# Kernel tuning notes

Hardware: AMD Instinct MI355X
Metric: run time of the kernel (lower is better)

Reference implementation:

```python
import jax, jax.numpy as jnp
import numpy as np

B, M, F = 32, 32768, 256


def setup_inputs() -> dict:
    key = jax.random.key(0)
    ks = jax.random.split(key, 6)
    scale1 = 1.0 / np.sqrt(2 * F)
    scale2 = 1.0 / np.sqrt(F)
    return {
        "input_data": jax.random.normal(ks[0], (B, F), dtype=jnp.float32),
        "memory": jax.random.normal(ks[1], (M, F), dtype=jnp.float32),
        "W1": jax.random.uniform(ks[2], (F, 2 * F), jnp.float32, -scale1, scale1),
        "b1": jax.random.uniform(ks[3], (F,), jnp.float32, -scale1, scale1),
        "W2": jax.random.uniform(ks[4], (1, F), jnp.float32, -scale2, scale2),
        "b2": jax.random.uniform(ks[5], (1,), jnp.float32, -scale2, scale2),
        # threshold below 1/M so the conditional scatter-write path actually fires
        # (torch default 0.05 with random weights never writes for M=32768)
        "threshold": jnp.float32(1e-5),
    }


def reference(input_data, memory, W1, b1, W2, b2, threshold):
    # Linear on cat([x, mem]) splits into two independent matmuls.
    W1x, W1m = W1[:, :F], W1[:, F:]          # each [F, F]
    hx = input_data @ W1x.T                   # [B, F]
    hm = memory @ W1m.T                       # [M, F]
    h = jnp.tanh(hx[:, None, :] + hm[None, :, :] + b1)  # [B, M, F]
    scores = h @ W2[0] + b2[0]                # [B, M]
    weights = jax.nn.softmax(scores, axis=1)  # softmax over memory slots
    best = jnp.argmax(weights, axis=1)        # [B] winning slot per item
    maxw = jnp.max(weights, axis=1)           # [B]
    mask = maxw > threshold                   # write only if above threshold
    # Sequential loop semantics: later batch items overwrite earlier ones
    # at the same slot. last[s] = 1 + index of last masked writer to slot s.
    order = jnp.where(mask, jnp.arange(B, dtype=jnp.int32) + 1, 0)
    last = jax.ops.segment_max(order, best, num_segments=M)  # [M]
    last = jnp.maximum(last, 0)
    src = input_data[jnp.maximum(last - 1, 0)]               # [M, F]
    updated_memory = jnp.where((last > 0)[:, None], src, memory)
    return updated_memory
```

## Files before the change

### kernel.cpp

```cpp
#include <hip/hip_runtime.h>

#define FDIM 256
#define BDIM 32
#define MDIM 32768
#define NB   512

#define WS_EM    0
#define WS_EX    (WS_EM + MDIM*FDIM)
#define WS_W2N   (WS_EX + BDIM*FDIM)
#define WS_PMAX  (WS_W2N + FDIM)
#define WS_PSUM  (WS_PMAX + BDIM*NB)
#define WS_PARG  (WS_PSUM + BDIM*NB)
#define WS_WIN   (WS_PARG + BDIM*NB)
#define WS_BEST  (WS_WIN + 32)
#define WS_GMAX  (WS_BEST + 32)
#define WS_GSUM  (WS_GMAX + 32)
#define WS_GARG  (WS_GSUM + 32)
#define WS_WH    (WS_GARG + 32)
#define WS_WL    (WS_WH + 32768)

#define C2 2.8853900817779268f

typedef __attribute__((ext_vector_type(8))) short bf16x8;
typedef __attribute__((ext_vector_type(8))) unsigned short ushort8;
typedef __attribute__((ext_vector_type(4))) float f32x4;

__device__ inline unsigned short f2bf(float x) {
  unsigned u = __float_as_uint(x);
  return (unsigned short)((u + 0x7fffu + ((u >> 16) & 1u)) >> 16);
}
__device__ inline float bf2f(unsigned short h) {
  return __uint_as_float(((unsigned)h) << 16);
}

__global__ __launch_bounds__(256) void k1_prep(const float* __restrict__ input,
                                               const float* __restrict__ W1,
                                               const float* __restrict__ b1,
                                               const float* __restrict__ W2,
                                               float* __restrict__ Ex,
                                               float* __restrict__ w2n,
                                               unsigned short* __restrict__ wh,
                                               unsigned short* __restrict__ wl) {
  if (blockIdx.x < BDIM) {
    const int b = blockIdx.x, f = threadIdx.x;
    const float* in = input + b * FDIM;
    const float* w  = W1 + (size_t)f * 512;
    float acc = b1[f];
    #pragma unroll 8
    for (int k = 0; k < FDIM; k += 4) {
      float4 iv = *(const float4*)(in + k);
      float4 wv = *(const float4*)(w + k);
      acc = fmaf(iv.x, wv.x, acc); acc = fmaf(iv.y, wv.y, acc);
      acc = fmaf(iv.z, wv.z, acc); acc = fmaf(iv.w, wv.w, acc);
    }
    Ex[b * FDIM + f] = __builtin_amdgcn_exp2f(acc * C2);
    if (b == 0) w2n[f] = -2.0f * W2[f];
  } else {
    int id = ((blockIdx.x - BDIM) * 256 + threadIdx.x) * 4;
    int f = id >> 8, c = id & 255;
    float4 v = *(const float4*)(W1 + (size_t)f * 512 + 256 + c);
    float xs[4] = {v.x, v.y, v.z, v.w};
    #pragma unroll
    for (int e = 0; e < 4; ++e) {
      unsigned short h = f2bf(xs[e]);
      wh[id + e] = h;
      wl[id + e] = f2bf(xs[e] - bf2f(h));
    }
  }
}

__global__ __launch_bounds__(512, 4) void k23_fused(const float* __restrict__ mem,
                                                    const unsigned short* __restrict__ wh,
                                                    const unsigned short* __restrict__ wl,
                                                    const float* __restrict__ Ex,
                                                    const float* __restrict__ w2n,
                                                    float* __restrict__ pmax,
                                                    float* __restrict__ psum,
                                                    int* __restrict__ parg,
                                                    float* __restrict__ out) {
  __shared__ __align__(16) char smem[69632];
  unsigned short* AH = (unsigned short*)(smem);
  unsigned short* AL = (unsigned short*)(smem + 5120);
  unsigned short* BH = (unsigned short*)(smem + 10240);
  unsigned short* BL = (unsigned short*)(smem + 30720);
  float* emT = (float*)smem;

  const int tid = threadIdx.x;
  const int lane = tid & 63, wid = tid >> 6;
  const int m0 = blockIdx.x * 64;
  const int rb = lane & 15, g8 = (lane >> 4) * 8;
  const int mh = wid & 1;
  const int fq = wid >> 1;

  float4 pa0, pa1;
  uint4  pb[8];
  const int ar = tid >> 2, ac8 = (tid & 3) * 8;
  const int bt2 = tid - 256;

  auto LOADS = [&](int s) {
    const int k0 = s * 32;
    if (tid < 256) {
      const float* mrow = mem + (size_t)(m0 + ar) * 256 + k0 + ac8;
      pa0 = *(const float4*)(mrow);
      pa1 = *(const float4*)(mrow + 4);
    } else {
      #pragma unroll
      for (int q = 0; q < 4; ++q) {
        int id = q * 256 + bt2, br = id >> 2, bc = (id & 3) * 8;
        pb[q * 2 + 0] = *(const uint4*)(wh + (size_t)br * 256 + k0 + bc);
        pb[q * 2 + 1] = *(const uint4*)(wl + (size_t)br * 256 + k0 + bc);
      }
    }
  };

  auto WRITES = [&](int s) {
    const int k0 = s * 32;
    if (tid < 256) {
      float* orow = out + (size_t)(m0 + ar) * 256 + k0 + ac8;
      *(float4*)(orow)     = pa0;
      *(float4*)(orow + 4) = pa1;
      float xs[8] = {pa0.x, pa0.y, pa0.z, pa0.w, pa1.x, pa1.y, pa1.z, pa1.w};
      ushort8 ahv, alv;
      #pragma unroll
      for (int e = 0; e < 8; ++e) {
        unsigned short h = f2bf(xs[e]);
        ahv[e] = h;
        alv[e] = f2bf(xs[e] - bf2f(h));
      }
      *(ushort8*)&AH[ar * 40 + ac8] = ahv;
      *(ushort8*)&AL[ar * 40 + ac8] = alv;
    } else {
      #pragma unroll
      for (int q = 0; q < 4; ++q) {
        int id = q * 256 + bt2, br = id >> 2, bc = (id & 3) * 8;
        *(uint4*)&BH[br * 40 + bc] = pb[q * 2 + 0];
        *(uint4*)&BL[br * 40 + bc] = pb[q * 2 + 1];
      }
    }
  };

  f32x4 acc[2][4];
  #pragma unroll
  for (int i = 0; i < 2; ++i)
    #pragma unroll
    for (int j = 0; j < 4; ++j) acc[i][j] = (f32x4){0.f, 0.f, 0.f, 0.f};

  LOADS(0);
  for (int s = 0; s < 8; ++s) {
    __syncthreads();
    WRITES(s);
    __syncthreads();
    if (s < 7) LOADS(s + 1);

    bf16x8 fah[2], fal[2], fbh[4], fbl[4];
    #pragma unroll
    for (int i = 0; i < 2; ++i) {
      fah[i] = *(const bf16x8*)&AH[(mh * 32 + i * 16 + rb) * 40 + g8];
      fal[i] = *(const bf16x8*)&AL[(mh * 32 + i * 16 + rb) * 40 + g8];
    }
    #pragma unroll
    for (int j = 0; j < 4; ++j) {
      fbh[j] = *(const bf16x8*)&BH[(fq * 64 + j * 16 + rb) * 40 + g8];
      fbl[j] = *(const bf16x8*)&BL[(fq * 64 + j * 16 + rb) * 40 + g8];
    }
    #pragma unroll
    for (int i = 0; i < 2; ++i)
      #pragma unroll
      for (int j = 0; j < 4; ++j) {
        acc[i][j] = __builtin_amdgcn_mfma_f32_16x16x32_bf16(fah[i], fbh[j], acc[i][j], 0, 0, 0);
        acc[i][j] = __builtin_amdgcn_mfma_f32_16x16x32_bf16(fah[i], fbl[j], acc[i][j], 0, 0, 0);
        acc[i][j] = __builtin_amdgcn_mfma_f32_16x16x32_bf16(fal[i], fbh[j], acc[i][j], 0, 0, 0);
      }
  }

  __syncthreads();
  #pragma unroll
  for (int j = 0; j < 4; ++j)
    #pragma unroll
    for (int i = 0; i < 2; ++i) {
      const int fl = fq * 64 + j * 16 + rb;
      const int mloc = mh * 32 + i * 16 + (lane >> 4) * 4;
      float4 v;
      v.x = __builtin_amdgcn_exp2f(acc[i][j][0] * C2);
      v.y = __builtin_amdgcn_exp2f(acc[i][j][1] * C2);
      v.z = __builtin_amdgcn_exp2f(acc[i][j][2] * C2);
      v.w = __builtin_amdgcn_exp2f(acc[i][j][3] * C2);
      *(float4*)(emT + fl * 68 + mloc) = v;
    }
  __syncthreads();

  const int wuid = __builtin_amdgcn_readfirstlane(wid);
  const float* ex0 = Ex + (size_t)(wuid * 4 + 0) * FDIM;
  const float* ex1 = Ex + (size_t)(wuid * 4 + 1) * FDIM;
  const float* ex2 = Ex + (size_t)(wuid * 4 + 2) * FDIM;
  const float* ex3 = Ex + (size_t)(wuid * 4 + 3) * FDIM;

  float acc0 = 0.f, acc1 = 0.f, acc2 = 0.f, acc3 = 0.f;
  #pragma unroll 2
  for (int f = 0; f < FDIM; f += 4) {
    float e0 = emT[(f + 0) * 68 + lane];
    float e1 = emT[(f + 1) * 68 + lane];
    float e2 = emT[(f + 2) * 68 + lane];
    float e3 = emT[(f + 3) * 68 + lane];
    float w0 = w2n[f + 0], w1 = w2n[f + 1];
    float w2 = w2n[f + 2], w3 = w2n[f + 3];
    #define SCORE4(exP, accV)                                            \
    {                                                                    \
      float u0 = fmaf(e0, exP[f + 0], 1.f);                              \
      float u1 = fmaf(e1, exP[f + 1], 1.f);                              \
      float u2 = fmaf(e2, exP[f + 2], 1.f);                              \
      float u3 = fmaf(e3, exP[f + 3], 1.f);                              \
      float p01 = u0 * u1, p23 = u2 * u3;                                \
      float den = p01 * p23;                                             \
      float t0 = fmaf(w1, u0, w0 * u1);                                  \
      float t1 = fmaf(w3, u2, w2 * u3);                                  \
      float num = fmaf(t1, p01, t0 * p23);                               \
      accV = fmaf(num, __builtin_amdgcn_rcpf(den), accV);                \
    }
    SCORE4(ex0, acc0)
    SCORE4(ex1, acc1)
    SCORE4(ex2, acc2)
    SCORE4(ex3, acc3)
    #undef SCORE4
  }

  float accb[4] = {acc0, acc1, acc2, acc3};
  const int blk = blockIdx.x;
  #pragma unroll
  for (int bi = 0; bi < 4; ++bi) {
    float s = accb[bi]; int idx = m0 + lane;
    #pragma unroll
    for (int off = 32; off > 0; off >>= 1) {
      float so = __shfl_xor(s, off);
      int   io = __shfl_xor(idx, off);
      if (so > s || (so == s && io < idx)) { s = so; idx = io; }
    }
    float ex = __expf(accb[bi] - s);
    #pragma unroll
    for (int off = 32; off > 0; off >>= 1) ex += __shfl_xor(ex, off);
    if (lane == 0) {
      int b = wuid * 4 + bi;
      pmax[b * NB + blk] = s;
      psum[b * NB + blk] = ex;
      parg[b * NB + blk] = idx;
    }
  }
}

__global__ __launch_bounds__(256) void k4a_reduce(const float* __restrict__ pmax,
                                                  const float* __restrict__ psum,
                                                  const int* __restrict__ parg,
                                                  float* __restrict__ gmax,
                                                  float* __restrict__ gsum,
                                                  int* __restrict__ garg) {
  __shared__ float sm[4], ss[4];
  __shared__ int   sa[4];
  const int b = blockIdx.x, tid = threadIdx.x;
  float cm = -3.0e38f, cs = 0.f; int ca = 0x7fffffff;
  #pragma unroll
  for (int t = 0; t < NB / 256; ++t) {
    int i = t * 256 + tid;
    float s = pmax[b * NB + i];
    float p = psum[b * NB + i];
    int   a = parg[b * NB + i];
    if (s > cm)      { cs = cs * __expf(cm - s) + p; cm = s; ca = a; }
    else if (s == cm){ cs += p; if (a < ca) ca = a; }
    else             { cs += p * __expf(s - cm); }
  }
  #pragma unroll
  for (int off = 32; off > 0; off >>= 1) {
    float om = __shfl_xor(cm, off);
    float os = __shfl_xor(cs, off);
    int   oa = __shfl_xor(ca, off);
    if (om > cm)      { cs = cs * __expf(cm - om) + os; cm = om; ca = oa; }
    else if (om == cm){ cs += os; if (oa < ca) ca = oa; }
    else              { cs += os * __expf(om - cm); }
  }
  if ((tid & 63) == 0) { sm[tid >> 6] = cm; ss[tid >> 6] = cs; sa[tid >> 6] = ca; }
  __syncthreads();
  if (tid == 0) {
    cm = sm[0]; cs = ss[0]; ca = sa[0];
    for (int w = 1; w < 4; ++w) {
      float om = sm[w], os = ss[w]; int oa = sa[w];
      if (om > cm)      { cs = cs * __expf(cm - om) + os; cm = om; ca = oa; }
      else if (om == cm){ cs += os; if (oa < ca) ca = oa; }
      else              { cs += os * __expf(om - cm); }
    }
    gmax[b] = cm; gsum[b] = cs; garg[b] = ca;
  }
}

__global__ __launch_bounds__(64) void k5_select_patch(const float* __restrict__ gsum,
                                                      const int* __restrict__ garg,
                                                      const float* __restrict__ thr_p,
                                                      const float* __restrict__ input,
                                                      float* __restrict__ out) {
  const int b = blockIdx.x;
  const float thr = *thr_p;
  const int me = garg[b];
  int w = (1.0f / gsum[b] > thr) ? 1 : 0;
  if (w) {
    for (int b2 = b + 1; b2 < BDIM; ++b2)
      if ((1.0f / gsum[b2] > thr) && garg[b2] == me) { w = 0; break; }
  }
  if (!w) return;
  const int t = threadIdx.x;
  *(float4*)(out + (size_t)me * 256 + t * 4) = *(const float4*)(input + (size_t)b * 256 + t * 4);
}

extern "C" void kernel_launch(void* const* d_in, const int* in_sizes, int n_in,
                              void* d_out, int out_size, void* d_ws, size_t ws_size,
                              hipStream_t stream) {
  const float* input  = (const float*)d_in[0];
  const float* memory = (const float*)d_in[1];
  const float* W1     = (const float*)d_in[2];
  const float* b1     = (const float*)d_in[3];
  const float* W2     = (const float*)d_in[4];
  const float* thr    = (const float*)d_in[6];

  float* ws   = (float*)d_ws;
  float* Ex   = ws + WS_EX;
  float* w2n  = ws + WS_W2N;
  float* pmax = ws + WS_PMAX;
  float* psum = ws + WS_PSUM;
  int*   parg = (int*)(ws + WS_PARG);
  float* gmax = ws + WS_GMAX;
  float* gsum = ws + WS_GSUM;
  int*   garg = (int*)(ws + WS_GARG);
  unsigned short* wh = (unsigned short*)(ws + WS_WH);
  unsigned short* wl = (unsigned short*)(ws + WS_WL);
  float* out  = (float*)d_out;

  hipLaunchKernelGGL(k1_prep,    dim3(BDIM + 64), dim3(256), 0, stream, input, W1, b1, W2, Ex, w2n, wh, wl);
  hipLaunchKernelGGL(k23_fused,  dim3(MDIM / 64), dim3(512), 0, stream, memory, wh, wl, Ex, w2n, pmax, psum, parg, out);
  hipLaunchKernelGGL(k4a_reduce, dim3(BDIM),      dim3(256), 0, stream, pmax, psum, parg, gmax, gsum, garg);
  hipLaunchKernelGGL(k5_select_patch, dim3(BDIM), dim3(64),  0, stream, gsum, garg, thr, input, out);
}
```

Measured before the change: 87.53 us.

## Load W1m tiles directly to LDS with swizzle and overlap staging with MFMA

Replaces register-staged B-operand (weight hi/lo bf16) loads with global_load_lds direct-to-LDS transfers, using an XOR swizzled unpadded layout to avoid bank conflicts. The main loop is restructured so fragments are read first, then a barrier, then the next k-slice's LDS writes and global loads are issued before the MFMAs, with a waitcnt+barrier after. This is meant to overlap memory staging with compute and free registers, at the cost of hand-managed waitcnt/barrier correctness and reliance on single-buffered LDS reuse.

```diff
diff --git a/kernel.cpp b/kernel.cpp
--- a/kernel.cpp
+++ b/kernel.cpp
@@ -24,6 +24,13 @@
 typedef __attribute__((ext_vector_type(8))) short bf16x8;
 typedef __attribute__((ext_vector_type(8))) unsigned short ushort8;
 typedef __attribute__((ext_vector_type(4))) float f32x4;
+
+#define AS1 __attribute__((address_space(1)))
+#define AS3 __attribute__((address_space(3)))
+
+__device__ __forceinline__ void gload16(const void* g, void* l) {
+  __builtin_amdgcn_global_load_lds((const AS1 void*)g, (AS3 void*)l, 16, 0, 0);
+}
 
 __device__ inline unsigned short f2bf(float x) {
   unsigned u = __float_as_uint(x);
@@ -81,8 +88,8 @@
   __shared__ __align__(16) char smem[69632];
   unsigned short* AH = (unsigned short*)(smem);
   unsigned short* AL = (unsigned short*)(smem + 5120);
-  unsigned short* BH = (unsigned short*)(smem + 10240);
-  unsigned short* BL = (unsigned short*)(smem + 30720);
+  char* BHb = smem + 10240;
+  char* BLb = smem + 26624;
   float* emT = (float*)smem;
 
   const int tid = threadIdx.x;
@@ -92,52 +99,44 @@
   const int mh = wid & 1;
   const int fq = wid >> 1;
 
+  const int ar = tid >> 2, ac8 = (tid & 3) * 8;
+  const int iw = wid - 4;
+  const int brow_l = lane >> 2, bbo = (lane & 3) * 16;
+
   float4 pa0, pa1;
-  uint4  pb[8];
-  const int ar = tid >> 2, ac8 = (tid & 3) * 8;
-  const int bt2 = tid - 256;
-
-  auto LOADS = [&](int s) {
-    const int k0 = s * 32;
-    if (tid < 256) {
-      const float* mrow = mem + (size_t)(m0 + ar) * 256 + k0 + ac8;
-      pa0 = *(const float4*)(mrow);
-      pa1 = *(const float4*)(mrow + 4);
-    } else {
-      #pragma unroll
-      for (int q = 0; q < 4; ++q) {
-        int id = q * 256 + bt2, br = id >> 2, bc = (id & 3) * 8;
-        pb[q * 2 + 0] = *(const uint4*)(wh + (size_t)br * 256 + k0 + bc);
-        pb[q * 2 + 1] = *(const uint4*)(wl + (size_t)br * 256 + k0 + bc);
-      }
-    }
-  };
-
-  auto WRITES = [&](int s) {
-    const int k0 = s * 32;
-    if (tid < 256) {
-      float* orow = out + (size_t)(m0 + ar) * 256 + k0 + ac8;
-      *(float4*)(orow)     = pa0;
-      *(float4*)(orow + 4) = pa1;
-      float xs[8] = {pa0.x, pa0.y, pa0.z, pa0.w, pa1.x, pa1.y, pa1.z, pa1.w};
-      ushort8 ahv, alv;
-      #pragma unroll
-      for (int e = 0; e < 8; ++e) {
-        unsigned short h = f2bf(xs[e]);
-        ahv[e] = h;
-        alv[e] = f2bf(xs[e] - bf2f(h));
-      }
-      *(ushort8*)&AH[ar * 40 + ac8] = ahv;
-      *(ushort8*)&AL[ar * 40 + ac8] = alv;
-    } else {
-      #pragma unroll
-      for (int q = 0; q < 4; ++q) {
-        int id = q * 256 + bt2, br = id >> 2, bc = (id & 3) * 8;
-        *(uint4*)&BH[br * 40 + bc] = pb[q * 2 + 0];
-        *(uint4*)&BL[br * 40 + bc] = pb[q * 2 + 1];
-      }
-    }
-  };
+
+  if (tid < 256) {
+    const float* mrow = mem + (size_t)(m0 + ar) * 256 + ac8;
+    float4 a0 = *(const float4*)(mrow);
+    float4 a1 = *(const float4*)(mrow + 4);
+    float* orow = out + (size_t)(m0 + ar) * 256 + ac8;
+    *(float4*)(orow)     = a0;
+    *(float4*)(orow + 4) = a1;
+    float xs[8] = {a0.x, a0.y, a0.z, a0.w, a1.x, a1.y, a1.z, a1.w};
+    ushort8 ahv, alv;
+    #pragma unroll
+    for (int e = 0; e < 8; ++e) {
+      unsigned short h = f2bf(xs[e]);
+      ahv[e] = h;
+      alv[e] = f2bf(xs[e] - bf2f(h));
+    }
+    *(ushort8*)&AH[ar * 40 + ac8] = ahv;
+    *(ushort8*)&AL[ar * 40 + ac8] = alv;
+    const float* mrow1 = mem + (size_t)(m0 + ar) * 256 + 32 + ac8;
+    pa0 = *(const float4*)(mrow1);
+    pa1 = *(const float4*)(mrow1 + 4);
+  } else {
+    #pragma unroll
+    for (int q = 0; q < 4; ++q) {
+      const int c = iw * 4 + q;
+      const int row = c * 16 + brow_l;
+      const int sbo = bbo ^ (((row >> 1) & 3) << 4);
+      gload16(wh + (size_t)row * 256 + (sbo >> 1), BHb + c * 1024);
+      gload16(wl + (size_t)row * 256 + (sbo >> 1), BLb + c * 1024);
+    }
+    asm volatile("s_waitcnt vmcnt(0)" ::: "memory");
+  }
+  __syncthreads();
 
   f32x4 acc[2][4];
   #pragma unroll
@@ -145,13 +144,7 @@
     #pragma unroll
     for (int j = 0; j < 4; ++j) acc[i][j] = (f32x4){0.f, 0.f, 0.f, 0.f};
 
-  LOADS(0);
   for (int s = 0; s < 8; ++s) {
-    __syncthreads();
-    WRITES(s);
-    __syncthreads();
-    if (s < 7) LOADS(s + 1);
-
     bf16x8 fah[2], fal[2], fbh[4], fbl[4];
     #pragma unroll
     for (int i = 0; i < 2; ++i) {
@@ -160,9 +153,49 @@
     }
     #pragma unroll
     for (int j = 0; j < 4; ++j) {
-      fbh[j] = *(const bf16x8*)&BH[(fq * 64 + j * 16 + rb) * 40 + g8];
-      fbl[j] = *(const bf16x8*)&BL[(fq * 64 + j * 16 + rb) * 40 + g8];
-    }
+      const int row = fq * 64 + j * 16 + rb;
+      const int bo  = (g8 * 2) ^ (((row >> 1) & 3) << 4);
+      fbh[j] = *(const bf16x8*)(BHb + row * 64 + bo);
+      fbl[j] = *(const bf16x8*)(BLb + row * 64 + bo);
+    }
+    asm volatile("s_waitcnt lgkmcnt(0)" ::: "memory");
+    __builtin_amdgcn_sched_barrier(0);
+    __builtin_amdgcn_s_barrier();
+    __builtin_amdgcn_sched_barrier(0);
+
+    if (s < 7) {
+      const int k1o = (s + 1) * 32;
+      if (tid < 256) {
+        float xs[8] = {pa0.x, pa0.y, pa0.z, pa0.w, pa1.x, pa1.y, pa1.z, pa1.w};
+        ushort8 ahv, alv;
+        #pragma unroll
+        for (int e = 0; e < 8; ++e) {
+          unsigned short h = f2bf(xs[e]);
+          ahv[e] = h;
+          alv[e] = f2bf(xs[e] - bf2f(h));
+        }
+        *(ushort8*)&AH[ar * 40 + ac8] = ahv;
+        *(ushort8*)&AL[ar * 40 + ac8] = alv;
+        float* orow = out + (size_t)(m0 + ar) * 256 + k1o + ac8;
+        *(float4*)(orow)     = pa0;
+        *(float4*)(orow + 4) = pa1;
+        if (s < 6) {
+          const float* mrow = mem + (size_t)(m0 + ar) * 256 + k1o + 32 + ac8;
+          pa0 = *(const float4*)(mrow);
+          pa1 = *(const float4*)(mrow + 4);
+        }
+      } else {
+        #pragma unroll
+        for (int q = 0; q < 4; ++q) {
+          const int c = iw * 4 + q;
+          const int row = c * 16 + brow_l;
+          const int sbo = bbo ^ (((row >> 1) & 3) << 4);
+          gload16(wh + (size_t)row * 256 + k1o + (sbo >> 1), BHb + c * 1024);
+          gload16(wl + (size_t)row * 256 + k1o + (sbo >> 1), BLb + c * 1024);
+        }
+      }
+    }
+
     #pragma unroll
     for (int i = 0; i < 2; ++i)
       #pragma unroll
@@ -171,6 +204,17 @@
         acc[i][j] = __builtin_amdgcn_mfma_f32_16x16x32_bf16(fah[i], fbl[j], acc[i][j], 0, 0, 0);
         acc[i][j] = __builtin_amdgcn_mfma_f32_16x16x32_bf16(fal[i], fbh[j], acc[i][j], 0, 0, 0);
       }
+
+    if (s < 7) {
+      if (tid < 256) {
+        asm volatile("s_waitcnt lgkmcnt(0)" ::: "memory");
+      } else {
+        asm volatile("s_waitcnt vmcnt(0)" ::: "memory");
+      }
+      __builtin_amdgcn_sched_barrier(0);
+      __builtin_amdgcn_s_barrier();
+      __builtin_amdgcn_sched_barrier(0);
+    }
   }
 
   __syncthreads();
```

Result: faster. 75.59 us (-13.6%).
